# Performance work log

Measured on AMD Instinct MI355X. Metric: run time of the kernel, lower is better.

Reference implementation:

```python
import jax, jax.numpy as jnp
import numpy as np

NUM_LEVELS = 8
BASE_RES = 32
MAX_RES = 2048
FEAT_DIM = 8
MAX_TABLE = 2 ** 19
WIDTH = 256
DEPTH = 8
NUM_FREQS = 4
N = 1048576

RESOLUTIONS = [min(BASE_RES * 2 ** l, MAX_RES) for l in range(NUM_LEVELS)]
TABLE_SIZES = [min(r ** 3, MAX_TABLE) for r in RESOLUTIONS]
POS_DIM = NUM_LEVELS * FEAT_DIM            # 64
VIEW_DIM = 3 + 3 * 2 * NUM_FREQS          # 27
IN_DIM = POS_DIM + VIEW_DIM                # 91


def _xavier(key, shape):
    fan_in, fan_out = shape[-2], shape[-1]
    limit = float(np.sqrt(6.0 / (fan_in + fan_out)))
    return jax.random.uniform(key, shape, jnp.float32, -limit, limit)


def setup_inputs() -> dict:
    key = jax.random.key(0)
    ks = jax.random.split(key, 32)
    inp = {
        'positions': jax.random.uniform(ks[0], (N, 3), jnp.float32),  # in [0,1) subset of [-1,1]
        'viewdirs': jax.random.normal(ks[1], (N, 3), jnp.float32),
    }
    for l in range(NUM_LEVELS):
        inp[f'table{l}'] = _xavier(ks[2 + l], (TABLE_SIZES[l], FEAT_DIM))
    inp['w0'] = _xavier(ks[12], (IN_DIM, WIDTH))
    inp['b0'] = jnp.zeros((WIDTH,), jnp.float32)
    # 6 hidden (with ReLU) + 1 final (no ReLU) 256x256 linears, stacked
    inp['wh'] = _xavier(ks[13], (DEPTH - 1, WIDTH, WIDTH))
    inp['bh'] = jnp.zeros((DEPTH - 1, WIDTH), jnp.float32)
    inp['wd'] = _xavier(ks[14], (WIDTH, 1))
    inp['bd'] = jnp.zeros((1,), jnp.float32)
    inp['wc'] = _xavier(ks[15], (WIDTH, 3))
    inp['bc'] = jnp.zeros((3,), jnp.float32)
    return inp


def _hash_encode(positions, table, res):
    # (p + 1) * 0.5 * res, clamped to [0, res-1]
    ps = jnp.clip((positions + 1.0) * (0.5 * res), 0.0, res - 1.0)
    idx_f = ps[..., 0] * (res * res) + ps[..., 1] * res + ps[..., 2]
    # clamp in float first so int32 cast is safe (matches torch clamp-to-table)
    idx = jnp.clip(idx_f, 0.0, table.shape[0] - 1.0).astype(jnp.int32)
    return table[idx]  # [..., FEAT_DIM]


def _view_encode(v):
    feats = [v]
    for f in range(NUM_FREQS):
        feats.append(jnp.sin((2.0 ** f) * jnp.pi * v))
        feats.append(jnp.cos((2.0 ** f) * jnp.pi * v))
    return jnp.concatenate(feats, axis=-1)


def reference(positions, viewdirs, table0, table1, table2, table3, table4,
              table5, table6, table7, w0, b0, wh, bh, wd, bd, wc, bc):
    tables = [table0, table1, table2, table3, table4, table5, table6, table7]
    spatial = jnp.concatenate(
        [_hash_encode(positions, tables[l], RESOLUTIONS[l]) for l in range(NUM_LEVELS)],
        axis=-1)                                           # [N, 64]
    feats = jnp.concatenate([spatial, _view_encode(viewdirs)], axis=-1)  # [N, 91]

    x = jax.nn.relu(feats @ w0 + b0)
    for i in range(DEPTH - 2):                             # 6 hidden layers with ReLU
        x = jax.nn.relu(x @ wh[i] + bh[i])
    x = x @ wh[DEPTH - 2] + bh[DEPTH - 2]                  # final linear, no ReLU

    density = x @ wd + bd                                  # [N, 1]
    color = jax.nn.sigmoid(x @ wc + bc)                    # [N, 3]
    return density, color
```

## Files before the change

### kernel.cpp

```cpp
#include <hip/hip_runtime.h>
#include <math.h>

#define N_PTS 1048576

typedef _Float16 half8 __attribute__((ext_vector_type(8)));
typedef _Float16 half4v __attribute__((ext_vector_type(4)));
typedef float float4v __attribute__((ext_vector_type(4)));
typedef float f32x16 __attribute__((ext_vector_type(16)));

#define W0T_OFF 0
#define WHT_OFF 24576
#define WHEAD_OFF 483328
#define WS_HALVES 487424

__global__ void prep_weights(const float* __restrict__ w0,
                             const float* __restrict__ wh,
                             const float* __restrict__ wd,
                             const float* __restrict__ wc,
                             _Float16* __restrict__ ws) {
  int stride = gridDim.x * blockDim.x;
  for (int i = blockIdx.x * blockDim.x + threadIdx.x; i < WS_HALVES; i += stride) {
    float v;
    if (i < WHT_OFF) {
      int kb = i >> 11, n = (i >> 3) & 255, j = i & 7;
      int k = kb * 8 + j;
      v = (k < 91) ? w0[k * 256 + n] : 0.0f;
    } else if (i < WHEAD_OFF) {
      int rel = i - WHT_OFF;
      int layer = rel >> 16;
      int r = rel & 65535;
      int kb = r >> 11, n = (r >> 3) & 255, j = r & 7;
      int k = kb * 8 + j;
      v = wh[(layer << 16) + k * 256 + n];
    } else {
      int rel = i - WHEAD_OFF;
      int n = rel >> 8, k = rel & 255;
      v = (n == 0) ? wd[k] : ((n < 4) ? wc[k * 3 + n - 1] : 0.0f);
    }
    ws[i] = (_Float16)v;
  }
}

#define BIAS_LDS 65536
__device__ __forceinline__ int x2addr(int m, int kb) {
  return (m >> 5) * 16384 + kb * 512 + (m & 31) * 16;
}

template <int KB>
__device__ __forceinline__ void mlp_layer(char* X, const _Float16* __restrict__ Wt,
                                          const _Float16* __restrict__ Wt_next,
                                          size_t laneoff, int bias_off, bool relu,
                                          int wn, int lr5, int lg2,
                                          half8& a0, half8& a1) {
  const _Float16* wb = Wt + laneoff;
  const _Float16* wbn = Wt_next + laneoff;
  const int broff = lg2 * 512 + lr5 * 16;

  half8 bc0 = *(const half8*)&X[broff];
  half8 bc1 = *(const half8*)&X[broff + 16384];
  half8 bc2 = *(const half8*)&X[broff + 32768];
  half8 bc3 = *(const half8*)&X[broff + 49152];
  float4v bq[2][4];
#pragma unroll
  for (int nt = 0; nt < 2; ++nt)
#pragma unroll
    for (int q = 0; q < 4; ++q)
      bq[nt][q] = *(const float4v*)&X[bias_off +
                                      (wn * 64 + nt * 32 + q * 8 + lg2 * 4) * 4];

  f32x16 acc[2][4];
#pragma unroll
  for (int nt = 0; nt < 2; ++nt)
#pragma unroll
    for (int q = 0; q < 4; ++q)
#pragma unroll
      for (int mt = 0; mt < 4; ++mt)
#pragma unroll
        for (int rr = 0; rr < 4; ++rr) acc[nt][mt][q * 4 + rr] = bq[nt][q][rr];

#pragma unroll
  for (int ks = 0; ks < KB; ++ks) {
    const _Float16* nb = (ks + 1 < KB) ? (wb + (size_t)(ks + 1) * 4096) : wbn;
    half8 a0n = *(const half8*)nb;
    half8 a1n = *(const half8*)(nb + 256);
    half8 bn0 = bc0, bn1 = bc1, bn2 = bc2, bn3 = bc3;
    if (ks + 1 < KB) {
      const int c = broff + (ks + 1) * 1024;
      bn0 = *(const half8*)&X[c];
      bn1 = *(const half8*)&X[c + 16384];
      bn2 = *(const half8*)&X[c + 32768];
      bn3 = *(const half8*)&X[c + 49152];
    }
    __builtin_amdgcn_s_setprio(1);
    acc[0][0] = __builtin_amdgcn_mfma_f32_32x32x16_f16(a0, bc0, acc[0][0], 0, 0, 0);
    acc[1][0] = __builtin_amdgcn_mfma_f32_32x32x16_f16(a1, bc0, acc[1][0], 0, 0, 0);
    acc[0][1] = __builtin_amdgcn_mfma_f32_32x32x16_f16(a0, bc1, acc[0][1], 0, 0, 0);
    acc[1][1] = __builtin_amdgcn_mfma_f32_32x32x16_f16(a1, bc1, acc[1][1], 0, 0, 0);
    acc[0][2] = __builtin_amdgcn_mfma_f32_32x32x16_f16(a0, bc2, acc[0][2], 0, 0, 0);
    acc[1][2] = __builtin_amdgcn_mfma_f32_32x32x16_f16(a1, bc2, acc[1][2], 0, 0, 0);
    acc[0][3] = __builtin_amdgcn_mfma_f32_32x32x16_f16(a0, bc3, acc[0][3], 0, 0, 0);
    acc[1][3] = __builtin_amdgcn_mfma_f32_32x32x16_f16(a1, bc3, acc[1][3], 0, 0, 0);
    __builtin_amdgcn_s_setprio(0);
    a0 = a0n; a1 = a1n;
    bc0 = bn0; bc1 = bn1; bc2 = bn2; bc3 = bn3;
  }
  __syncthreads();

  const half4v zero4 = {(_Float16)0, (_Float16)0, (_Float16)0, (_Float16)0};
#pragma unroll
  for (int mt = 0; mt < 4; ++mt) {
#pragma unroll
    for (int nt = 0; nt < 2; ++nt)
#pragma unroll
      for (int q = 0; q < 4; ++q) {
        half4v hv;
#pragma unroll
        for (int rr = 0; rr < 4; ++rr) hv[rr] = (_Float16)acc[nt][mt][q * 4 + rr];
        if (relu) hv = __builtin_elementwise_max(hv, zero4);
        *(half4v*)&X[mt * 16384 + (wn * 8 + nt * 4 + q) * 512 + lr5 * 16 + lg2 * 8] = hv;
      }
  }
  __syncthreads();
}

__global__ __launch_bounds__(256, 2) void nerf_fused(
    const float* __restrict__ pos, const float* __restrict__ vdir,
    const float* __restrict__ t0, const float* __restrict__ t1,
    const float* __restrict__ t2, const float* __restrict__ t3,
    const float* __restrict__ t4, const float* __restrict__ t5,
    const float* __restrict__ t6, const float* __restrict__ t7,
    const float* __restrict__ b0, const float* __restrict__ bh,
    const float* __restrict__ bd, const float* __restrict__ bc,
    const _Float16* __restrict__ ws, float* __restrict__ out) {
  __shared__ __align__(16) char X[73728];
  const int tid = threadIdx.x;
  const int wg = blockIdx.x;
  const int m = tid & 127;
  const int p = wg * 128 + m;

  const int lane = tid & 63;
  const int w = tid >> 6;
  const int lr5 = lane & 31;
  const int lg2 = lane >> 5;
  const size_t laneoff = ((size_t)(lg2 * 256 + w * 64 + lr5)) * 8;

  half8 a0 = *(const half8*)(ws + W0T_OFF + laneoff);
  half8 a1 = *(const half8*)(ws + W0T_OFF + laneoff + 256);

  if (tid < 128) {
    const float px = pos[p * 3], py = pos[p * 3 + 1], pz = pos[p * 3 + 2];
    const float* tabs[8] = {t0, t1, t2, t3, t4, t5, t6, t7};
    const int resi[8] = {32, 64, 128, 256, 512, 1024, 2048, 2048};
    const float tmax[8] = {32767.0f, 262143.0f, 524287.0f, 524287.0f,
                           524287.0f, 524287.0f, 524287.0f, 524287.0f};
#pragma unroll
    for (int lv = 0; lv < 8; ++lv) {
      const float r = (float)resi[lv];
      const float hr = 0.5f * r;
      const float rm1 = r - 1.0f;
      float cx = fminf(fmaxf(__fmul_rn(__fadd_rn(px, 1.0f), hr), 0.0f), rm1);
      float cy = fminf(fmaxf(__fmul_rn(__fadd_rn(py, 1.0f), hr), 0.0f), rm1);
      float cz = fminf(fmaxf(__fmul_rn(__fadd_rn(pz, 1.0f), hr), 0.0f), rm1);
      float idxf = __fadd_rn(__fadd_rn(__fmul_rn(cx, r * r), __fmul_rn(cy, r)), cz);
      idxf = fminf(fmaxf(idxf, 0.0f), tmax[lv]);
      int idx = (int)idxf;
      const float4* row = (const float4*)(tabs[lv] + (size_t)idx * 8);
      float4 f0 = row[0], f1 = row[1];
      half8 h;
      h[0] = (_Float16)f0.x; h[1] = (_Float16)f0.y;
      h[2] = (_Float16)f0.z; h[3] = (_Float16)f0.w;
      h[4] = (_Float16)f1.x; h[5] = (_Float16)f1.y;
      h[6] = (_Float16)f1.z; h[7] = (_Float16)f1.w;
      *(half8*)&X[x2addr(m, lv)] = h;
    }
  } else {
    float v0 = vdir[p * 3], v1 = vdir[p * 3 + 1], v2 = vdir[p * 3 + 2];
    const float cf[4] = {(float)(M_PI), (float)(2.0 * M_PI),
                         (float)(4.0 * M_PI), (float)(8.0 * M_PI)};
    float feat[32];
    feat[0] = v0; feat[1] = v1; feat[2] = v2;
    float vv[3] = {v0, v1, v2};
#pragma unroll
    for (int f = 0; f < 4; ++f)
#pragma unroll
      for (int d = 0; d < 3; ++d) {
        float arg = __fmul_rn(cf[f], vv[d]);
        feat[3 + f * 6 + d] = __sinf(arg);
        feat[6 + f * 6 + d] = __cosf(arg);
      }
#pragma unroll
    for (int i = 27; i < 32; ++i) feat[i] = 0.0f;
#pragma unroll
    for (int s = 0; s < 4; ++s) {
      half8 h;
#pragma unroll
      for (int j = 0; j < 8; ++j) h[j] = (_Float16)feat[s * 8 + j];
      *(half8*)&X[x2addr(m, 8 + s)] = h;
    }
  }
#pragma unroll
  for (int i = 0; i < 8; ++i) {
    int idx = tid + i * 256;
    float bv = (idx < 256) ? b0[idx] : bh[idx - 256];
    *(float*)&X[BIAS_LDS + idx * 4] = bv;
  }
  __syncthreads();

  mlp_layer<6>(X, ws + W0T_OFF, ws + WHT_OFF, laneoff, BIAS_LDS, true,
               w, lr5, lg2, a0, a1);
#pragma unroll 1
  for (int i = 0; i < 7; ++i) {
    const _Float16* wnext =
        (i < 6) ? (ws + WHT_OFF + ((i + 1) << 16)) : (ws + W0T_OFF);
    mlp_layer<16>(X, ws + WHT_OFF + (i << 16), wnext, laneoff,
                  BIAS_LDS + (i + 1) * 1024, i < 6, w, lr5, lg2, a0, a1);
  }

  const int lr = lane & 15;
  const int lg = lane >> 4;
  float4v hacc[2];
  {
    float bv = (lr == 0) ? bd[0] : ((lr < 4) ? bc[lr - 1] : 0.0f);
    hacc[0] = (float4v){bv, bv, bv, bv};
    hacc[1] = hacc[0];
  }
  const _Float16* Wh = ws + WHEAD_OFF;
#pragma unroll
  for (int ks = 0; ks < 8; ++ks) {
    half8 bfr = *(const half8*)(Wh + lr * 256 + ks * 32 + lg * 8);
#pragma unroll
    for (int mt = 0; mt < 2; ++mt) {
      half8 a = *(const half8*)&X[x2addr(w * 32 + mt * 16 + lr, ks * 4 + lg)];
      hacc[mt] = __builtin_amdgcn_mfma_f32_16x16x32_f16(a, bfr, hacc[mt], 0, 0, 0);
    }
  }
#pragma unroll
  for (int mt = 0; mt < 2; ++mt)
#pragma unroll
    for (int r = 0; r < 4; ++r) {
      int pp = wg * 128 + w * 32 + mt * 16 + lg * 4 + r;
      float vv = hacc[mt][r];
      if (lr == 0) {
        out[pp] = vv;
      } else if (lr < 4) {
        out[N_PTS + 3 * pp + (lr - 1)] = 1.0f / (1.0f + __expf(-vv));
      }
    }
}

extern "C" void kernel_launch(void* const* d_in, const int* in_sizes, int n_in,
                              void* d_out, int out_size, void* d_ws, size_t ws_size,
                              hipStream_t stream) {
  const float* pos = (const float*)d_in[0];
  const float* vdir = (const float*)d_in[1];
  const float* t0 = (const float*)d_in[2];
  const float* t1 = (const float*)d_in[3];
  const float* t2 = (const float*)d_in[4];
  const float* t3 = (const float*)d_in[5];
  const float* t4 = (const float*)d_in[6];
  const float* t5 = (const float*)d_in[7];
  const float* t6 = (const float*)d_in[8];
  const float* t7 = (const float*)d_in[9];
  const float* w0 = (const float*)d_in[10];
  const float* b0 = (const float*)d_in[11];
  const float* wh = (const float*)d_in[12];
  const float* bh = (const float*)d_in[13];
  const float* wd = (const float*)d_in[14];
  const float* bd = (const float*)d_in[15];
  const float* wc = (const float*)d_in[16];
  const float* bc = (const float*)d_in[17];
  _Float16* ws = (_Float16*)d_ws;
  float* out = (float*)d_out;

  hipLaunchKernelGGL(prep_weights, dim3((WS_HALVES + 255) / 256), dim3(256), 0, stream,
                     w0, wh, wd, wc, ws);
  hipLaunchKernelGGL(nerf_fused, dim3(N_PTS / 128), dim3(256), 0, stream,
                     pos, vdir, t0, t1, t2, t3, t4, t5, t6, t7,
                     b0, bh, bd, bc, (const _Float16*)ws, out);
}
```

Before: 854.7 us.

## Shrink point tile to 96 rows to fit three workgroups per CU

Each workgroup now handles 96 points instead of 128. This cuts the LDS activation buffer to 48KB and the accumulator set to 2x3 tiles, so launch bounds can request three blocks per CU. Biases are read straight from global memory instead of being staged in LDS, and the hash-gather work is spread across all 256 threads, with the last block's tail handled by bounds guards. Per-block weight traffic now feeds fewer MFMAs, which lowers weight reuse in exchange for more occupancy to hide latency.

Result: slower. 928.1 us (+8.6%).

```diff
diff --git a/kernel.cpp b/kernel.cpp
--- a/kernel.cpp
+++ b/kernel.cpp
@@ -41,7 +41,6 @@
   }
 }
 
-#define BIAS_LDS 65536
 __device__ __forceinline__ int x2addr(int m, int kb) {
   return (m >> 5) * 16384 + kb * 512 + (m & 31) * 16;
 }
@@ -49,7 +48,8 @@
 template <int KB>
 __device__ __forceinline__ void mlp_layer(char* X, const _Float16* __restrict__ Wt,
                                           const _Float16* __restrict__ Wt_next,
-                                          size_t laneoff, int bias_off, bool relu,
+                                          size_t laneoff,
+                                          const float* __restrict__ bias, bool relu,
                                           int wn, int lr5, int lg2,
                                           half8& a0, half8& a1) {
   const _Float16* wb = Wt + laneoff;
@@ -59,22 +59,20 @@
   half8 bc0 = *(const half8*)&X[broff];
   half8 bc1 = *(const half8*)&X[broff + 16384];
   half8 bc2 = *(const half8*)&X[broff + 32768];
-  half8 bc3 = *(const half8*)&X[broff + 49152];
   float4v bq[2][4];
 #pragma unroll
   for (int nt = 0; nt < 2; ++nt)
 #pragma unroll
     for (int q = 0; q < 4; ++q)
-      bq[nt][q] = *(const float4v*)&X[bias_off +
-                                      (wn * 64 + nt * 32 + q * 8 + lg2 * 4) * 4];
-
-  f32x16 acc[2][4];
+      bq[nt][q] = *(const float4v*)(bias + wn * 64 + nt * 32 + q * 8 + lg2 * 4);
+
+  f32x16 acc[2][3];
 #pragma unroll
   for (int nt = 0; nt < 2; ++nt)
 #pragma unroll
     for (int q = 0; q < 4; ++q)
 #pragma unroll
-      for (int mt = 0; mt < 4; ++mt)
+      for (int mt = 0; mt < 3; ++mt)
 #pragma unroll
         for (int rr = 0; rr < 4; ++rr) acc[nt][mt][q * 4 + rr] = bq[nt][q][rr];
 
@@ -83,13 +81,12 @@
     const _Float16* nb = (ks + 1 < KB) ? (wb + (size_t)(ks + 1) * 4096) : wbn;
     half8 a0n = *(const half8*)nb;
     half8 a1n = *(const half8*)(nb + 256);
-    half8 bn0 = bc0, bn1 = bc1, bn2 = bc2, bn3 = bc3;
+    half8 bn0 = bc0, bn1 = bc1, bn2 = bc2;
     if (ks + 1 < KB) {
       const int c = broff + (ks + 1) * 1024;
       bn0 = *(const half8*)&X[c];
       bn1 = *(const half8*)&X[c + 16384];
       bn2 = *(const half8*)&X[c + 32768];
-      bn3 = *(const half8*)&X[c + 49152];
     }
     __builtin_amdgcn_s_setprio(1);
     acc[0][0] = __builtin_amdgcn_mfma_f32_32x32x16_f16(a0, bc0, acc[0][0], 0, 0, 0);
@@ -98,17 +95,15 @@
     acc[1][1] = __builtin_amdgcn_mfma_f32_32x32x16_f16(a1, bc1, acc[1][1], 0, 0, 0);
     acc[0][2] = __builtin_amdgcn_mfma_f32_32x32x16_f16(a0, bc2, acc[0][2], 0, 0, 0);
     acc[1][2] = __builtin_amdgcn_mfma_f32_32x32x16_f16(a1, bc2, acc[1][2], 0, 0, 0);
-    acc[0][3] = __builtin_amdgcn_mfma_f32_32x32x16_f16(a0, bc3, acc[0][3], 0, 0, 0);
-    acc[1][3] = __builtin_amdgcn_mfma_f32_32x32x16_f16(a1, bc3, acc[1][3], 0, 0, 0);
     __builtin_amdgcn_s_setprio(0);
     a0 = a0n; a1 = a1n;
-    bc0 = bn0; bc1 = bn1; bc2 = bn2; bc3 = bn3;
+    bc0 = bn0; bc1 = bn1; bc2 = bn2;
   }
   __syncthreads();
 
   const half4v zero4 = {(_Float16)0, (_Float16)0, (_Float16)0, (_Float16)0};
 #pragma unroll
-  for (int mt = 0; mt < 4; ++mt) {
+  for (int mt = 0; mt < 3; ++mt) {
 #pragma unroll
     for (int nt = 0; nt < 2; ++nt)
 #pragma unroll
@@ -123,7 +118,7 @@
   __syncthreads();
 }
 
-__global__ __launch_bounds__(256, 2) void nerf_fused(
+__global__ __launch_bounds__(256, 3) void nerf_fused(
     const float* __restrict__ pos, const float* __restrict__ vdir,
     const float* __restrict__ t0, const float* __restrict__ t1,
     const float* __restrict__ t2, const float* __restrict__ t3,
@@ -132,11 +127,9 @@
     const float* __restrict__ b0, const float* __restrict__ bh,
     const float* __restrict__ bd, const float* __restrict__ bc,
     const _Float16* __restrict__ ws, float* __restrict__ out) {
-  __shared__ __align__(16) char X[73728];
+  __shared__ __align__(16) char X[49152];
   const int tid = threadIdx.x;
   const int wg = blockIdx.x;
-  const int m = tid & 127;
-  const int p = wg * 128 + m;
 
   const int lane = tid & 63;
   const int w = tid >> 6;
@@ -147,14 +140,19 @@
   half8 a0 = *(const half8*)(ws + W0T_OFF + laneoff);
   half8 a1 = *(const half8*)(ws + W0T_OFF + laneoff + 256);
 
-  if (tid < 128) {
-    const float px = pos[p * 3], py = pos[p * 3 + 1], pz = pos[p * 3 + 2];
+  {
     const float* tabs[8] = {t0, t1, t2, t3, t4, t5, t6, t7};
     const int resi[8] = {32, 64, 128, 256, 512, 1024, 2048, 2048};
     const float tmax[8] = {32767.0f, 262143.0f, 524287.0f, 524287.0f,
                            524287.0f, 524287.0f, 524287.0f, 524287.0f};
 #pragma unroll
-    for (int lv = 0; lv < 8; ++lv) {
+    for (int it = 0; it < 3; ++it) {
+      const int t = tid + it * 256;
+      const int m = t % 96;
+      const int lv = t / 96;
+      int p = wg * 96 + m;
+      if (p >= N_PTS) p = N_PTS - 1;
+      const float px = pos[p * 3], py = pos[p * 3 + 1], pz = pos[p * 3 + 2];
       const float r = (float)resi[lv];
       const float hr = 0.5f * r;
       const float rm1 = r - 1.0f;
@@ -173,7 +171,11 @@
       h[6] = (_Float16)f1.z; h[7] = (_Float16)f1.w;
       *(half8*)&X[x2addr(m, lv)] = h;
     }
-  } else {
+  }
+  if (tid < 96) {
+    const int m = tid;
+    int p = wg * 96 + m;
+    if (p >= N_PTS) p = N_PTS - 1;
     float v0 = vdir[p * 3], v1 = vdir[p * 3 + 1], v2 = vdir[p * 3 + 2];
     const float cf[4] = {(float)(M_PI), (float)(2.0 * M_PI),
                          (float)(4.0 * M_PI), (float)(8.0 * M_PI)};
@@ -198,54 +200,52 @@
       *(half8*)&X[x2addr(m, 8 + s)] = h;
     }
   }
-#pragma unroll
-  for (int i = 0; i < 8; ++i) {
-    int idx = tid + i * 256;
-    float bv = (idx < 256) ? b0[idx] : bh[idx - 256];
-    *(float*)&X[BIAS_LDS + idx * 4] = bv;
-  }
   __syncthreads();
 
-  mlp_layer<6>(X, ws + W0T_OFF, ws + WHT_OFF, laneoff, BIAS_LDS, true,
+  mlp_layer<6>(X, ws + W0T_OFF, ws + WHT_OFF, laneoff, b0, true,
                w, lr5, lg2, a0, a1);
 #pragma unroll 1
   for (int i = 0; i < 7; ++i) {
     const _Float16* wnext =
         (i < 6) ? (ws + WHT_OFF + ((i + 1) << 16)) : (ws + W0T_OFF);
     mlp_layer<16>(X, ws + WHT_OFF + (i << 16), wnext, laneoff,
-                  BIAS_LDS + (i + 1) * 1024, i < 6, w, lr5, lg2, a0, a1);
-  }
-
-  const int lr = lane & 15;
-  const int lg = lane >> 4;
-  float4v hacc[2];
-  {
-    float bv = (lr == 0) ? bd[0] : ((lr < 4) ? bc[lr - 1] : 0.0f);
-    hacc[0] = (float4v){bv, bv, bv, bv};
-    hacc[1] = hacc[0];
-  }
-  const _Float16* Wh = ws + WHEAD_OFF;
-#pragma unroll
-  for (int ks = 0; ks < 8; ++ks) {
-    half8 bfr = *(const half8*)(Wh + lr * 256 + ks * 32 + lg * 8);
-#pragma unroll
-    for (int mt = 0; mt < 2; ++mt) {
-      half8 a = *(const half8*)&X[x2addr(w * 32 + mt * 16 + lr, ks * 4 + lg)];
-      hacc[mt] = __builtin_amdgcn_mfma_f32_16x16x32_f16(a, bfr, hacc[mt], 0, 0, 0);
-    }
-  }
-#pragma unroll
-  for (int mt = 0; mt < 2; ++mt)
-#pragma unroll
-    for (int r = 0; r < 4; ++r) {
-      int pp = wg * 128 + w * 32 + mt * 16 + lg * 4 + r;
-      float vv = hacc[mt][r];
-      if (lr == 0) {
-        out[pp] = vv;
-      } else if (lr < 4) {
-        out[N_PTS + 3 * pp + (lr - 1)] = 1.0f / (1.0f + __expf(-vv));
-      }
-    }
+                  bh + (i << 8), i < 6, w, lr5, lg2, a0, a1);
+  }
+
+  if (w < 3) {
+    const int lr = lane & 15;
+    const int lg = lane >> 4;
+    float4v hacc[2];
+    {
+      float bv = (lr == 0) ? bd[0] : ((lr < 4) ? bc[lr - 1] : 0.0f);
+      hacc[0] = (float4v){bv, bv, bv, bv};
+      hacc[1] = hacc[0];
+    }
+    const _Float16* Wh = ws + WHEAD_OFF;
+#pragma unroll
+    for (int ks = 0; ks < 8; ++ks) {
+      half8 bfr = *(const half8*)(Wh + lr * 256 + ks * 32 + lg * 8);
+#pragma unroll
+      for (int mt = 0; mt < 2; ++mt) {
+        half8 a = *(const half8*)&X[x2addr(w * 32 + mt * 16 + lr, ks * 4 + lg)];
+        hacc[mt] = __builtin_amdgcn_mfma_f32_16x16x32_f16(a, bfr, hacc[mt], 0, 0, 0);
+      }
+    }
+#pragma unroll
+    for (int mt = 0; mt < 2; ++mt)
+#pragma unroll
+      for (int r = 0; r < 4; ++r) {
+        int pp = wg * 96 + w * 32 + mt * 16 + lg * 4 + r;
+        if (pp < N_PTS) {
+          float vv = hacc[mt][r];
+          if (lr == 0) {
+            out[pp] = vv;
+          } else if (lr < 4) {
+            out[N_PTS + 3 * pp + (lr - 1)] = 1.0f / (1.0f + __expf(-vv));
+          }
+        }
+      }
+  }
 }
 
 extern "C" void kernel_launch(void* const* d_in, const int* in_sizes, int n_in,
@@ -274,7 +274,7 @@
 
   hipLaunchKernelGGL(prep_weights, dim3((WS_HALVES + 255) / 256), dim3(256), 0, stream,
                      w0, wh, wd, wc, ws);
-  hipLaunchKernelGGL(nerf_fused, dim3(N_PTS / 128), dim3(256), 0, stream,
+  hipLaunchKernelGGL(nerf_fused, dim3((N_PTS + 95) / 96), dim3(256), 0, stream,
                      pos, vdir, t0, t1, t2, t3, t4, t5, t6, t7,
                      b0, bh, bd, bc, (const _Float16*)ws, out);
 }
```

## Split each block's MLP rows across two wave groups with 512-thread blocks

Applied to the files above, without the earlier changes.

Doubles the block to 512 threads (8 waves) and splits the 128-point M dimension between two groups of four waves. Each wave now keeps half the accumulators and issues half the MFMAs per k-step, which is meant to cut per-wave register pressure and give more waves to hide LDS and global latency. The trade-off is that weight fragments are now loaded redundantly by both wave groups. The launch bound also rises to 512 threads with 4 blocks, which may force a tight VGPR budget and cause spills, even though LDS use limits residency to fewer blocks anyway.

New measurement: 1.011 ms. 1.18x slower.

```diff
diff --git a/kernel.cpp b/kernel.cpp
--- a/kernel.cpp
+++ b/kernel.cpp
@@ -50,16 +50,14 @@
 __device__ __forceinline__ void mlp_layer(char* X, const _Float16* __restrict__ Wt,
                                           const _Float16* __restrict__ Wt_next,
                                           size_t laneoff, int bias_off, bool relu,
-                                          int wn, int lr5, int lg2,
+                                          int wn, int wm, int lr5, int lg2,
                                           half8& a0, half8& a1) {
   const _Float16* wb = Wt + laneoff;
   const _Float16* wbn = Wt_next + laneoff;
-  const int broff = lg2 * 512 + lr5 * 16;
+  const int broff = wm * 32768 + lg2 * 512 + lr5 * 16;
 
   half8 bc0 = *(const half8*)&X[broff];
   half8 bc1 = *(const half8*)&X[broff + 16384];
-  half8 bc2 = *(const half8*)&X[broff + 32768];
-  half8 bc3 = *(const half8*)&X[broff + 49152];
   float4v bq[2][4];
 #pragma unroll
   for (int nt = 0; nt < 2; ++nt)
@@ -68,13 +66,13 @@
       bq[nt][q] = *(const float4v*)&X[bias_off +
                                       (wn * 64 + nt * 32 + q * 8 + lg2 * 4) * 4];
 
-  f32x16 acc[2][4];
+  f32x16 acc[2][2];
 #pragma unroll
   for (int nt = 0; nt < 2; ++nt)
 #pragma unroll
     for (int q = 0; q < 4; ++q)
 #pragma unroll
-      for (int mt = 0; mt < 4; ++mt)
+      for (int mt = 0; mt < 2; ++mt)
 #pragma unroll
         for (int rr = 0; rr < 4; ++rr) acc[nt][mt][q * 4 + rr] = bq[nt][q][rr];
 
@@ -83,32 +81,26 @@
     const _Float16* nb = (ks + 1 < KB) ? (wb + (size_t)(ks + 1) * 4096) : wbn;
     half8 a0n = *(const half8*)nb;
     half8 a1n = *(const half8*)(nb + 256);
-    half8 bn0 = bc0, bn1 = bc1, bn2 = bc2, bn3 = bc3;
+    half8 bn0 = bc0, bn1 = bc1;
     if (ks + 1 < KB) {
       const int c = broff + (ks + 1) * 1024;
       bn0 = *(const half8*)&X[c];
       bn1 = *(const half8*)&X[c + 16384];
-      bn2 = *(const half8*)&X[c + 32768];
-      bn3 = *(const half8*)&X[c + 49152];
     }
     __builtin_amdgcn_s_setprio(1);
     acc[0][0] = __builtin_amdgcn_mfma_f32_32x32x16_f16(a0, bc0, acc[0][0], 0, 0, 0);
     acc[1][0] = __builtin_amdgcn_mfma_f32_32x32x16_f16(a1, bc0, acc[1][0], 0, 0, 0);
     acc[0][1] = __builtin_amdgcn_mfma_f32_32x32x16_f16(a0, bc1, acc[0][1], 0, 0, 0);
     acc[1][1] = __builtin_amdgcn_mfma_f32_32x32x16_f16(a1, bc1, acc[1][1], 0, 0, 0);
-    acc[0][2] = __builtin_amdgcn_mfma_f32_32x32x16_f16(a0, bc2, acc[0][2], 0, 0, 0);
-    acc[1][2] = __builtin_amdgcn_mfma_f32_32x32x16_f16(a1, bc2, acc[1][2], 0, 0, 0);
-    acc[0][3] = __builtin_amdgcn_mfma_f32_32x32x16_f16(a0, bc3, acc[0][3], 0, 0, 0);
-    acc[1][3] = __builtin_amdgcn_mfma_f32_32x32x16_f16(a1, bc3, acc[1][3], 0, 0, 0);
     __builtin_amdgcn_s_setprio(0);
     a0 = a0n; a1 = a1n;
-    bc0 = bn0; bc1 = bn1; bc2 = bn2; bc3 = bn3;
+    bc0 = bn0; bc1 = bn1;
   }
   __syncthreads();
 
   const half4v zero4 = {(_Float16)0, (_Float16)0, (_Float16)0, (_Float16)0};
 #pragma unroll
-  for (int mt = 0; mt < 4; ++mt) {
+  for (int mt = 0; mt < 2; ++mt) {
 #pragma unroll
     for (int nt = 0; nt < 2; ++nt)
 #pragma unroll
@@ -117,13 +109,14 @@
 #pragma unroll
         for (int rr = 0; rr < 4; ++rr) hv[rr] = (_Float16)acc[nt][mt][q * 4 + rr];
         if (relu) hv = __builtin_elementwise_max(hv, zero4);
-        *(half4v*)&X[mt * 16384 + (wn * 8 + nt * 4 + q) * 512 + lr5 * 16 + lg2 * 8] = hv;
+        *(half4v*)&X[(wm * 2 + mt) * 16384 + (wn * 8 + nt * 4 + q) * 512 +
+                     lr5 * 16 + lg2 * 8] = hv;
       }
   }
   __syncthreads();
 }
 
-__global__ __launch_bounds__(256, 2) void nerf_fused(
+__global__ __launch_bounds__(512, 4) void nerf_fused(
     const float* __restrict__ pos, const float* __restrict__ vdir,
     const float* __restrict__ t0, const float* __restrict__ t1,
     const float* __restrict__ t2, const float* __restrict__ t3,
@@ -140,9 +133,11 @@
 
   const int lane = tid & 63;
   const int w = tid >> 6;
+  const int wn = w & 3;
+  const int wm = w >> 2;
   const int lr5 = lane & 31;
   const int lg2 = lane >> 5;
-  const size_t laneoff = ((size_t)(lg2 * 256 + w * 64 + lr5)) * 8;
+  const size_t laneoff = ((size_t)(lg2 * 256 + wn * 64 + lr5)) * 8;
 
   half8 a0 = *(const half8*)(ws + W0T_OFF + laneoff);
   half8 a1 = *(const half8*)(ws + W0T_OFF + laneoff + 256);
@@ -173,7 +168,7 @@
       h[6] = (_Float16)f1.z; h[7] = (_Float16)f1.w;
       *(half8*)&X[x2addr(m, lv)] = h;
     }
-  } else {
+  } else if (tid < 256) {
     float v0 = vdir[p * 3], v1 = vdir[p * 3 + 1], v2 = vdir[p * 3 + 2];
     const float cf[4] = {(float)(M_PI), (float)(2.0 * M_PI),
                          (float)(4.0 * M_PI), (float)(8.0 * M_PI)};
@@ -199,53 +194,47 @@
     }
   }
 #pragma unroll
-  for (int i = 0; i < 8; ++i) {
-    int idx = tid + i * 256;
+  for (int i = 0; i < 4; ++i) {
+    int idx = tid + i * 512;
     float bv = (idx < 256) ? b0[idx] : bh[idx - 256];
     *(float*)&X[BIAS_LDS + idx * 4] = bv;
   }
   __syncthreads();
 
   mlp_layer<6>(X, ws + W0T_OFF, ws + WHT_OFF, laneoff, BIAS_LDS, true,
-               w, lr5, lg2, a0, a1);
+               wn, wm, lr5, lg2, a0, a1);
 #pragma unroll 1
   for (int i = 0; i < 7; ++i) {
     const _Float16* wnext =
         (i < 6) ? (ws + WHT_OFF + ((i + 1) << 16)) : (ws + W0T_OFF);
     mlp_layer<16>(X, ws + WHT_OFF + (i << 16), wnext, laneoff,
-                  BIAS_LDS + (i + 1) * 1024, i < 6, w, lr5, lg2, a0, a1);
+                  BIAS_LDS + (i + 1) * 1024, i < 6, wn, wm, lr5, lg2, a0, a1);
   }
 
   const int lr = lane & 15;
   const int lg = lane >> 4;
-  float4v hacc[2];
+  float4v hacc;
   {
     float bv = (lr == 0) ? bd[0] : ((lr < 4) ? bc[lr - 1] : 0.0f);
-    hacc[0] = (float4v){bv, bv, bv, bv};
-    hacc[1] = hacc[0];
+    hacc = (float4v){bv, bv, bv, bv};
   }
   const _Float16* Wh = ws + WHEAD_OFF;
 #pragma unroll
   for (int ks = 0; ks < 8; ++ks) {
     half8 bfr = *(const half8*)(Wh + lr * 256 + ks * 32 + lg * 8);
-#pragma unroll
-    for (int mt = 0; mt < 2; ++mt) {
-      half8 a = *(const half8*)&X[x2addr(w * 32 + mt * 16 + lr, ks * 4 + lg)];
-      hacc[mt] = __builtin_amdgcn_mfma_f32_16x16x32_f16(a, bfr, hacc[mt], 0, 0, 0);
-    }
-  }
-#pragma unroll
-  for (int mt = 0; mt < 2; ++mt)
-#pragma unroll
-    for (int r = 0; r < 4; ++r) {
-      int pp = wg * 128 + w * 32 + mt * 16 + lg * 4 + r;
-      float vv = hacc[mt][r];
-      if (lr == 0) {
-        out[pp] = vv;
-      } else if (lr < 4) {
-        out[N_PTS + 3 * pp + (lr - 1)] = 1.0f / (1.0f + __expf(-vv));
-      }
-    }
+    half8 a = *(const half8*)&X[x2addr(w * 16 + lr, ks * 4 + lg)];
+    hacc = __builtin_amdgcn_mfma_f32_16x16x32_f16(a, bfr, hacc, 0, 0, 0);
+  }
+#pragma unroll
+  for (int r = 0; r < 4; ++r) {
+    int pp = wg * 128 + w * 16 + lg * 4 + r;
+    float vv = hacc[r];
+    if (lr == 0) {
+      out[pp] = vv;
+    } else if (lr < 4) {
+      out[N_PTS + 3 * pp + (lr - 1)] = 1.0f / (1.0f + __expf(-vv));
+    }
+  }
 }
 
 extern "C" void kernel_launch(void* const* d_in, const int* in_sizes, int n_in,
@@ -274,7 +263,7 @@
 
   hipLaunchKernelGGL(prep_weights, dim3((WS_HALVES + 255) / 256), dim3(256), 0, stream,
                      w0, wh, wd, wc, ws);
-  hipLaunchKernelGGL(nerf_fused, dim3(N_PTS / 128), dim3(256), 0, stream,
+  hipLaunchKernelGGL(nerf_fused, dim3(N_PTS / 128), dim3(512), 0, stream,
                      pos, vdir, t0, t1, t2, t3, t4, t5, t6, t7,
                      b0, bh, bd, bc, (const _Float16*)ws, out);
 }
```

## Switch MLP wave tiling to 2x2 split over rows and output columns

Applied to the files above, without the earlier changes.

Each wave now computes 128 output columns for 64 points instead of 64 columns for all 128 points. This halves the LDS activation fragment reads per wave per k-step and doubles the per-wave weight fragment loads from global memory. The goal is to relieve LDS bandwidth pressure in the MFMA loop. The cost is more global/L2 weight traffic and two extra prefetched weight registers per wave.

Measured after the change: 899.8 us. +5.3%, slower.

```diff
diff --git a/kernel.cpp b/kernel.cpp
--- a/kernel.cpp
+++ b/kernel.cpp
@@ -50,74 +50,69 @@
 __device__ __forceinline__ void mlp_layer(char* X, const _Float16* __restrict__ Wt,
                                           const _Float16* __restrict__ Wt_next,
                                           size_t laneoff, int bias_off, bool relu,
-                                          int wn, int lr5, int lg2,
-                                          half8& a0, half8& a1) {
+                                          int wn, int wm, int lr5, int lg2,
+                                          half8& a0, half8& a1, half8& a2, half8& a3) {
   const _Float16* wb = Wt + laneoff;
   const _Float16* wbn = Wt_next + laneoff;
-  const int broff = lg2 * 512 + lr5 * 16;
+  const int broff = wm * 32768 + lg2 * 512 + lr5 * 16;
 
   half8 bc0 = *(const half8*)&X[broff];
   half8 bc1 = *(const half8*)&X[broff + 16384];
-  half8 bc2 = *(const half8*)&X[broff + 32768];
-  half8 bc3 = *(const half8*)&X[broff + 49152];
-  float4v bq[2][4];
-#pragma unroll
-  for (int nt = 0; nt < 2; ++nt)
-#pragma unroll
-    for (int q = 0; q < 4; ++q)
-      bq[nt][q] = *(const float4v*)&X[bias_off +
-                                      (wn * 64 + nt * 32 + q * 8 + lg2 * 4) * 4];
-
-  f32x16 acc[2][4];
-#pragma unroll
-  for (int nt = 0; nt < 2; ++nt)
-#pragma unroll
-    for (int q = 0; q < 4; ++q)
-#pragma unroll
-      for (int mt = 0; mt < 4; ++mt)
-#pragma unroll
-        for (int rr = 0; rr < 4; ++rr) acc[nt][mt][q * 4 + rr] = bq[nt][q][rr];
+
+  f32x16 acc[4][2];
+#pragma unroll
+  for (int nt = 0; nt < 4; ++nt)
+#pragma unroll
+    for (int q = 0; q < 4; ++q) {
+      float4v bv = *(const float4v*)&X[bias_off +
+                                       (wn * 128 + nt * 32 + q * 8 + lg2 * 4) * 4];
+#pragma unroll
+      for (int mt = 0; mt < 2; ++mt)
+#pragma unroll
+        for (int rr = 0; rr < 4; ++rr) acc[nt][mt][q * 4 + rr] = bv[rr];
+    }
 
 #pragma unroll
   for (int ks = 0; ks < KB; ++ks) {
     const _Float16* nb = (ks + 1 < KB) ? (wb + (size_t)(ks + 1) * 4096) : wbn;
     half8 a0n = *(const half8*)nb;
     half8 a1n = *(const half8*)(nb + 256);
-    half8 bn0 = bc0, bn1 = bc1, bn2 = bc2, bn3 = bc3;
+    half8 a2n = *(const half8*)(nb + 512);
+    half8 a3n = *(const half8*)(nb + 768);
+    half8 bn0 = bc0, bn1 = bc1;
     if (ks + 1 < KB) {
       const int c = broff + (ks + 1) * 1024;
       bn0 = *(const half8*)&X[c];
       bn1 = *(const half8*)&X[c + 16384];
-      bn2 = *(const half8*)&X[c + 32768];
-      bn3 = *(const half8*)&X[c + 49152];
     }
     __builtin_amdgcn_s_setprio(1);
     acc[0][0] = __builtin_amdgcn_mfma_f32_32x32x16_f16(a0, bc0, acc[0][0], 0, 0, 0);
     acc[1][0] = __builtin_amdgcn_mfma_f32_32x32x16_f16(a1, bc0, acc[1][0], 0, 0, 0);
+    acc[2][0] = __builtin_amdgcn_mfma_f32_32x32x16_f16(a2, bc0, acc[2][0], 0, 0, 0);
+    acc[3][0] = __builtin_amdgcn_mfma_f32_32x32x16_f16(a3, bc0, acc[3][0], 0, 0, 0);
     acc[0][1] = __builtin_amdgcn_mfma_f32_32x32x16_f16(a0, bc1, acc[0][1], 0, 0, 0);
     acc[1][1] = __builtin_amdgcn_mfma_f32_32x32x16_f16(a1, bc1, acc[1][1], 0, 0, 0);
-    acc[0][2] = __builtin_amdgcn_mfma_f32_32x32x16_f16(a0, bc2, acc[0][2], 0, 0, 0);
-    acc[1][2] = __builtin_amdgcn_mfma_f32_32x32x16_f16(a1, bc2, acc[1][2], 0, 0, 0);
-    acc[0][3] = __builtin_amdgcn_mfma_f32_32x32x16_f16(a0, bc3, acc[0][3], 0, 0, 0);
-    acc[1][3] = __builtin_amdgcn_mfma_f32_32x32x16_f16(a1, bc3, acc[1][3], 0, 0, 0);
+    acc[2][1] = __builtin_amdgcn_mfma_f32_32x32x16_f16(a2, bc1, acc[2][1], 0, 0, 0);
+    acc[3][1] = __builtin_amdgcn_mfma_f32_32x32x16_f16(a3, bc1, acc[3][1], 0, 0, 0);
     __builtin_amdgcn_s_setprio(0);
-    a0 = a0n; a1 = a1n;
-    bc0 = bn0; bc1 = bn1; bc2 = bn2; bc3 = bn3;
+    a0 = a0n; a1 = a1n; a2 = a2n; a3 = a3n;
+    bc0 = bn0; bc1 = bn1;
   }
   __syncthreads();
 
   const half4v zero4 = {(_Float16)0, (_Float16)0, (_Float16)0, (_Float16)0};
 #pragma unroll
-  for (int mt = 0; mt < 4; ++mt) {
-#pragma unroll
-    for (int nt = 0; nt < 2; ++nt)
+  for (int mt = 0; mt < 2; ++mt) {
+#pragma unroll
+    for (int nt = 0; nt < 4; ++nt)
 #pragma unroll
       for (int q = 0; q < 4; ++q) {
         half4v hv;
 #pragma unroll
         for (int rr = 0; rr < 4; ++rr) hv[rr] = (_Float16)acc[nt][mt][q * 4 + rr];
         if (relu) hv = __builtin_elementwise_max(hv, zero4);
-        *(half4v*)&X[mt * 16384 + (wn * 8 + nt * 4 + q) * 512 + lr5 * 16 + lg2 * 8] = hv;
+        *(half4v*)&X[(wm * 2 + mt) * 16384 + (wn * 16 + nt * 4 + q) * 512 +
+                     lr5 * 16 + lg2 * 8] = hv;
       }
   }
   __syncthreads();
@@ -140,12 +135,16 @@
 
   const int lane = tid & 63;
   const int w = tid >> 6;
+  const int wn = w & 1;
+  const int wm = w >> 1;
   const int lr5 = lane & 31;
   const int lg2 = lane >> 5;
-  const size_t laneoff = ((size_t)(lg2 * 256 + w * 64 + lr5)) * 8;
+  const size_t laneoff = ((size_t)(lg2 * 256 + wn * 128 + lr5)) * 8;
 
   half8 a0 = *(const half8*)(ws + W0T_OFF + laneoff);
   half8 a1 = *(const half8*)(ws + W0T_OFF + laneoff + 256);
+  half8 a2 = *(const half8*)(ws + W0T_OFF + laneoff + 512);
+  half8 a3 = *(const half8*)(ws + W0T_OFF + laneoff + 768);
 
   if (tid < 128) {
     const float px = pos[p * 3], py = pos[p * 3 + 1], pz = pos[p * 3 + 2];
@@ -207,13 +206,14 @@
   __syncthreads();
 
   mlp_layer<6>(X, ws + W0T_OFF, ws + WHT_OFF, laneoff, BIAS_LDS, true,
-               w, lr5, lg2, a0, a1);
+               wn, wm, lr5, lg2, a0, a1, a2, a3);
 #pragma unroll 1
   for (int i = 0; i < 7; ++i) {
     const _Float16* wnext =
         (i < 6) ? (ws + WHT_OFF + ((i + 1) << 16)) : (ws + W0T_OFF);
     mlp_layer<16>(X, ws + WHT_OFF + (i << 16), wnext, laneoff,
-                  BIAS_LDS + (i + 1) * 1024, i < 6, w, lr5, lg2, a0, a1);
+                  BIAS_LDS + (i + 1) * 1024, i < 6, wn, wm, lr5, lg2,
+                  a0, a1, a2, a3);
   }
 
   const int lr = lane & 15;
```
